# Kernel optimization log

Measured on AMD Instinct MI355X. Metric: run time of the kernel, lower is better.

The kernel has to match this reference:

```python
import jax, jax.numpy as jnp
import numpy as np

G = 4096              # number of graphs in batch
NPG = 198             # nodes per graph (fixed by view(-1, 198*2))
N = G * NPG           # total nodes = 811008
DEG = 8               # avg degree
E = N * DEG           # total edges = 6488064
CONV_DIMS = [(2, 20), (20, 15), (15, 10), (10, 5), (5, 2)]
MLP_DIMS = [(396, 200), (200, 100), (100, 50), (50, 10), (10, 2)]


def setup_inputs() -> dict:
    key = jax.random.key(0)
    ks = jax.random.split(key, 64)
    x = jax.random.normal(ks[0], (N, 2), dtype=jnp.float32)
    # block-diagonal edges: endpoints within each 198-node graph, then offset
    src = jax.random.randint(ks[1], (G, E // G), 0, NPG)
    dst = jax.random.randint(ks[2], (G, E // G), 0, NPG)
    off = (jnp.arange(G, dtype=jnp.int32) * NPG)[:, None]
    edge_index = jnp.stack([(src + off).reshape(-1), (dst + off).reshape(-1)]).astype(jnp.int32)
    edge_weight = jax.random.uniform(ks[3], (E,), dtype=jnp.float32)
    inp = {"x": x, "edge_index": edge_index, "edge_weight": edge_weight}
    ki = 4
    for i, (ci, co) in enumerate(CONV_DIMS):
        s = 1.0 / np.sqrt(ci)
        inp[f"w_rel{i}"] = jax.random.normal(ks[ki], (co, ci), jnp.float32) * s; ki += 1
        inp[f"b_rel{i}"] = jax.random.normal(ks[ki], (co,), jnp.float32) * s; ki += 1
        inp[f"w_root{i}"] = jax.random.normal(ks[ki], (co, ci), jnp.float32) * s; ki += 1
    for i, (ci, co) in enumerate(MLP_DIMS):
        s = 1.0 / np.sqrt(ci)
        inp[f"lw{i}"] = jax.random.normal(ks[ki], (co, ci), jnp.float32) * s; ki += 1
        inp[f"lb{i}"] = jax.random.normal(ks[ki], (co,), jnp.float32) * s; ki += 1
    return inp


def _graph_conv(x, src, dst, ew, w_rel, b_rel, w_root):
    # PyG GraphConv: lin_rel(sum_{j->i} e_ji * x_j) + lin_root(x_i)
    msg = x[src] * ew[:, None]                               # [E, Cin] gather
    agg = jax.ops.segment_sum(msg, dst, num_segments=N)      # [N, Cin] scatter-add
    return agg @ w_rel.T + b_rel + x @ w_root.T              # [N, Cout]


def reference(x, edge_index, edge_weight,
              w_rel0, b_rel0, w_root0, w_rel1, b_rel1, w_root1,
              w_rel2, b_rel2, w_root2, w_rel3, b_rel3, w_root3,
              w_rel4, b_rel4, w_root4,
              lw0, lb0, lw1, lb1, lw2, lb2, lw3, lb3, lw4, lb4):
    src, dst = edge_index[0], edge_index[1]
    convs = [(w_rel0, b_rel0, w_root0), (w_rel1, b_rel1, w_root1),
             (w_rel2, b_rel2, w_root2), (w_rel3, b_rel3, w_root3),
             (w_rel4, b_rel4, w_root4)]
    h = x
    for wr, br, wroot in convs:
        h = jax.nn.relu(_graph_conv(h, src, dst, edge_weight, wr, br, wroot))
    h = h.reshape(-1, NPG * 2)                               # [G, 396]
    mlp = [(lw0, lb0), (lw1, lb1), (lw2, lb2), (lw3, lb3)]
    for w, b in mlp:
        h = jax.nn.relu(h @ w.T + b)
    logits = h @ lw4.T + lb4                                 # [G, 2]
    return jax.nn.softmax(logits, axis=1)
```

## Files before the change

### kernel.cpp

```cpp
#include <hip/hip_runtime.h>
#include <hip/hip_fp16.h>

#define NG    4096
#define NPG   198
#define EPG   1584
#define ETOT  (NG * EPG)
#define SHW   12

#define BC2(u) __builtin_bit_cast(__half2, (u))

typedef _Float16 f16x4 __attribute__((ext_vector_type(4)));
typedef float    f32x4 __attribute__((ext_vector_type(4)));
typedef float    f32x2 __attribute__((ext_vector_type(2)));

#define H_F16S    (NG * 396)
#define WTB_SZ    114688
#define WTB1_OFF  83200
#define WTB2_OFF  106496
#define WTB3_OFF  113664
#define CPK_PAIRS 562

__global__ __launch_bounds__(256) void wtrans16_kernel(
    const float* __restrict__ w0, const float* __restrict__ w1,
    const float* __restrict__ w2, const float* __restrict__ w3,
    _Float16* __restrict__ wtb)
{
    const int idx = blockIdx.x * 256 + threadIdx.x;
    if (idx >= 2 * WTB_SZ) return;
    const int half = idx >= WTB_SZ;
    const int rel0 = idx - half * WTB_SZ;
    const float* w; int K, N, NPAD, rel;
    if (rel0 < 83200)       { w = w0; K = 396; N = 200; NPAD = 208; rel = rel0; }
    else if (rel0 < 106496) { w = w1; K = 200; N = 100; NPAD = 112; rel = rel0 - 83200; }
    else if (rel0 < 113664) { w = w2; K = 100; N = 50;  NPAD = 64;  rel = rel0 - 106496; }
    else                    { w = w3; K = 50;  N = 10;  NPAD = 16;  rel = rel0 - 113664; }
    const int span = NPAD * 16;
    const int kc = rel / span;
    const int r  = rel - kc * span;
    const int n  = r >> 4, ki = r & 15;
    const int k  = kc * 16 + ki;
    const float v = (n < N && k < K) ? w[n * K + k] : 0.f;
    const _Float16 hi = (_Float16)v;
    wtb[idx] = half ? (_Float16)(v - (float)hi) : hi;
}

__global__ __launch_bounds__(256) void wpackc_kernel(
    const float* wr0, const float* wq0, const float* wr1, const float* wq1,
    const float* wr2, const float* wq2, const float* wr3, const float* wq3,
    const float* wr4, const float* wq4, f32x2* __restrict__ cpk)
{
    const int idx = blockIdx.x * 256 + threadIdx.x;
    if (idx >= CPK_PAIRS) return;
    const float *wrel, *wroot; int COUT, CIN, MSP, base;
    if (idx < 40)       { wrel=wr0; wroot=wq0; COUT=20; CIN=2;  MSP=1;  base=0;   }
    else if (idx < 340) { wrel=wr1; wroot=wq1; COUT=15; CIN=20; MSP=10; base=40;  }
    else if (idx < 500) { wrel=wr2; wroot=wq2; COUT=10; CIN=15; MSP=8;  base=340; }
    else if (idx < 550) { wrel=wr3; wroot=wq3; COUT=5;  CIN=10; MSP=5;  base=500; }
    else                { wrel=wr4; wroot=wq4; COUT=2;  CIN=5;  MSP=3;  base=550; }
    const int r    = idx - base;
    const int half = r >= COUT * MSP;
    const int q    = r - half * COUT * MSP;
    const int o    = q / MSP, p = q - o * MSP;
    const float* w = half ? wroot : wrel;
    const int c0 = 2 * p, c1 = 2 * p + 1;
    f32x2 v;
    v.x = (c0 < CIN) ? w[o * CIN + c0] : 0.f;
    v.y = (c1 < CIN) ? w[o * CIN + c1] : 0.f;
    cpk[idx] = v;
}

template <int CIN, int COUT, int SIN, int SOUT>
__device__ __forceinline__ void conv_layer_h(
    const unsigned* __restrict__ h_in,
    unsigned* __restrict__ h_out,
    const unsigned* __restrict__ s_edge,
    const unsigned* __restrict__ row_start,
    const unsigned short* __restrict__ perm,
    const f32x2* __restrict__ wrelp,
    const f32x2* __restrict__ wrootp,
    const float* __restrict__ brel, int tid)
{
    if (tid >= NPG) return;
    const int node = (int)perm[tid];
    constexpr int MS = (CIN + 1) / 2;

    float aggf[MS * 2];
#pragma unroll
    for (int c = 0; c < MS * 2; ++c) aggf[c] = 0.f;

    const unsigned jb = row_start[node], je = row_start[node + 1];
    for (unsigned j = jb; j < je; ++j) {
        const unsigned e  = s_edge[j];
        const float    wf = __half2float(__ushort_as_half((unsigned short)(e >> 16)));
        const unsigned* row = h_in + (e & 0xFFFFu) * SIN;
        unsigned wv[MS];
        if constexpr (SIN == 1) {
            wv[0] = row[0];
        } else {
            const uint4 q0 = *(const uint4*)row;
            wv[0] = q0.x;
            if constexpr (MS > 1) wv[1] = q0.y;
            if constexpr (MS > 2) wv[2] = q0.z;
            if constexpr (MS > 3) wv[3] = q0.w;
            if constexpr (MS > 4) {
                const uint4 q1 = *(const uint4*)(row + 4);
                wv[4] = q1.x;
                if constexpr (MS > 5) wv[5] = q1.y;
                if constexpr (MS > 6) wv[6] = q1.z;
                if constexpr (MS > 7) wv[7] = q1.w;
            }
            if constexpr (MS > 8) {
                const uint4 q2 = *(const uint4*)(row + 8);
                wv[8] = q2.x;
                if constexpr (MS > 9) wv[9] = q2.y;
            }
        }
#pragma unroll
        for (int p = 0; p < MS; ++p) {
            const __half2 h2 = BC2(wv[p]);
            aggf[2*p]     = fmaf(wf, __low2float(h2),  aggf[2*p]);
            aggf[2*p + 1] = fmaf(wf, __high2float(h2), aggf[2*p + 1]);
        }
    }

    float hv[MS * 2];
    {
        const unsigned* me = h_in + node * SIN;
#pragma unroll
        for (int p = 0; p < MS; ++p) {
            const __half2 h2 = BC2(me[p]);
            hv[2*p]     = __low2float(h2);
            hv[2*p + 1] = __high2float(h2);
        }
    }

    float outv[COUT];
#pragma unroll
    for (int o = 0; o < COUT; ++o) {
        f32x2 acc; acc.x = brel[o]; acc.y = 0.f;
#pragma unroll
        for (int p = 0; p < MS; ++p) {
            f32x2 av; av.x = aggf[2*p]; av.y = aggf[2*p+1];
            acc = __builtin_elementwise_fma(av, wrelp[o * MS + p], acc);
            f32x2 hv2; hv2.x = hv[2*p]; hv2.y = hv[2*p+1];
            acc = __builtin_elementwise_fma(hv2, wrootp[o * MS + p], acc);
        }
        outv[o] = fmaxf(acc.x + acc.y, 0.f);
    }

    if constexpr (SOUT == 1) {
        h_out[node] = __builtin_bit_cast(unsigned,
            __floats2half2_rn(outv[0], COUT > 1 ? outv[1] : 0.f));
    } else {
        unsigned ow[SOUT];
#pragma unroll
        for (int p = 0; p < SOUT; ++p) {
            const float lo = (2 * p     < COUT) ? outv[2 * p]     : 0.f;
            const float hi = (2 * p + 1 < COUT) ? outv[2 * p + 1] : 0.f;
            ow[p] = __builtin_bit_cast(unsigned, __floats2half2_rn(lo, hi));
        }
        unsigned* orow = h_out + node * SOUT;
#pragma unroll
        for (int qn = 0; qn < SOUT / 4; ++qn)
            *(uint4*)(orow + 4 * qn) =
                make_uint4(ow[4*qn], ow[4*qn+1], ow[4*qn+2], ow[4*qn+3]);
    }
}

__global__ __launch_bounds__(256) void conv_kernel(
    const float* __restrict__ x,
    const int*   __restrict__ eidx,
    const float* __restrict__ ew,
    const f32x2* __restrict__ cpk,
    const float* __restrict__ br0, const float* __restrict__ br1,
    const float* __restrict__ br2, const float* __restrict__ br3,
    const float* __restrict__ br4,
    _Float16* __restrict__ H)
{
    __shared__ __align__(16) unsigned s_edge[EPG];
    __shared__ unsigned       cnt[256];
    __shared__ unsigned       cursor[256];
    __shared__ unsigned       row_start[NPG + 1];
    __shared__ unsigned       wsum[4];
    __shared__ unsigned       dhist[64];
    __shared__ unsigned       dcur[64];
    __shared__ unsigned short perm[NPG + 2];
    __shared__ __align__(16) unsigned bufA[NPG * SHW];
    __shared__ __align__(16) unsigned bufB[NPG * SHW];

    const int g = blockIdx.x, tid = threadIdx.x;
    const int ebase = g * EPG, nbase = g * NPG;
    const int lane = tid & 63, wid = tid >> 6;

    for (int i = tid; i < NPG * SHW; i += 256) { bufA[i] = 0u; bufB[i] = 0u; }

    const int4*   s4 = (const int4*)(eidx + ebase);
    const int4*   d4 = (const int4*)(eidx + ETOT + ebase);
    const float4* w4 = (const float4*)(ew + ebase);
    const int4   sa = s4[tid];
    const int4   da = d4[tid];
    const float4 wa = w4[tid];
    const bool hasb = tid < (EPG / 4 - 256);
    int4 sb = {0,0,0,0}, db = {0,0,0,0}; float4 wb = {0,0,0,0};
    if (hasb) { sb = s4[tid + 256]; db = d4[tid + 256]; wb = w4[tid + 256]; }

    cnt[tid] = 0u;
    __syncthreads();
    atomicAdd(&cnt[da.x - nbase], 1u); atomicAdd(&cnt[da.y - nbase], 1u);
    atomicAdd(&cnt[da.z - nbase], 1u); atomicAdd(&cnt[da.w - nbase], 1u);
    if (hasb) {
        atomicAdd(&cnt[db.x - nbase], 1u); atomicAdd(&cnt[db.y - nbase], 1u);
        atomicAdd(&cnt[db.z - nbase], 1u); atomicAdd(&cnt[db.w - nbase], 1u);
    }
    __syncthreads();

    const unsigned v = cnt[tid];
    unsigned inc = v;
#pragma unroll
    for (int s = 1; s < 64; s <<= 1) {
        const unsigned t = (unsigned)__shfl_up((int)inc, s);
        if (lane >= s) inc += t;
    }
    if (lane == 63) wsum[wid] = inc;
    __syncthreads();
    unsigned pre = 0;
    for (int w = 0; w < wid; ++w) pre += wsum[w];
    const unsigned excl = pre + inc - v;
    if (tid <= NPG) row_start[tid] = excl;
    if (tid < NPG)  cursor[tid]    = excl;
    __syncthreads();

    {
        auto place = [&](int s, int d, float w) {
            const int dl = d - nbase;
            const unsigned slot = atomicAdd(&cursor[dl], 1u);
            const __half hw = __float2half_rn(w);
            s_edge[slot] = ((unsigned)__half_as_ushort(hw) << 16)
                         | (unsigned)(s - nbase);
        };
        place(sa.x, da.x, wa.x); place(sa.y, da.y, wa.y);
        place(sa.z, da.z, wa.z); place(sa.w, da.w, wa.w);
        if (hasb) {
            place(sb.x, db.x, wb.x); place(sb.y, db.y, wb.y);
            place(sb.z, db.z, wb.z); place(sb.w, db.w, wb.w);
        }
    }

    if (tid < NPG) {
        const float2 xv = ((const float2*)x)[nbase + tid];
        bufA[tid] = __builtin_bit_cast(unsigned, __floats2half2_rn(xv.x, xv.y));
    }

    if (tid < 64) dhist[tid] = 0u;
    __syncthreads();
    unsigned mydeg = 0u;
    if (tid < NPG) {
        mydeg = v; if (mydeg > 63u) mydeg = 63u;
        atomicAdd(&dhist[mydeg], 1u);
    }
    __syncthreads();
    if (tid < 64) {
        const unsigned dv = dhist[tid];
        unsigned sc = dv;
#pragma unroll
        for (int s = 1; s < 64; s <<= 1) {
            const unsigned t = (unsigned)__shfl_up((int)sc, s);
            if (lane >= s) sc += t;
        }
        dcur[tid] = sc - dv;
    }
    __syncthreads();
    if (tid < NPG) {
        const unsigned pos = atomicAdd(&dcur[mydeg], 1u);
        perm[pos] = (unsigned short)tid;
    }
    __syncthreads();

    conv_layer_h<2,  20, 1,   SHW>(bufA, bufB, s_edge, row_start, perm,
                                   cpk + 0,   cpk + 20,        br0, tid);
    __syncthreads();
    conv_layer_h<20, 15, SHW, SHW>(bufB, bufA, s_edge, row_start, perm,
                                   cpk + 40,  cpk + 40 + 150,  br1, tid);
    __syncthreads();
    conv_layer_h<15, 10, SHW, SHW>(bufA, bufB, s_edge, row_start, perm,
                                   cpk + 340, cpk + 340 + 80,  br2, tid);
    __syncthreads();
    conv_layer_h<10, 5,  SHW, SHW>(bufB, bufA, s_edge, row_start, perm,
                                   cpk + 500, cpk + 500 + 25,  br3, tid);
    __syncthreads();
    conv_layer_h<5,  2,  SHW, 1  >(bufA, bufB, s_edge, row_start, perm,
                                   cpk + 550, cpk + 550 + 6,   br4, tid);
    __syncthreads();

    if (tid < NPG)
        ((unsigned*)H)[g * NPG + tid] = bufB[tid];
}

__device__ __forceinline__ void zero_words(void* p, int nwords, int tid)
{
    unsigned* u = (unsigned*)p;
    for (int i = tid; i < nwords; i += 512) u[i] = 0u;
}

template<int KC, int NTT, int NOUT, int SIN, int SOUT>
__device__ __forceinline__ void mfma_layer(
    const _Float16* __restrict__ inb,
    _Float16* __restrict__ outb,
    const _Float16* __restrict__ wthi,
    const _Float16* __restrict__ wtlo,
    const float* __restrict__ bias, int tid)
{
    constexpr int NPAD = NTT * 16;
    const int lane = tid & 63, wid = tid >> 6;
    const int lrow = lane & 15, lgrp = lane >> 4;
    const int nt0 = wid;
    if (nt0 >= NTT) return;
    const bool has2 = (nt0 + 8) < NTT;
    const _Float16* aptr = inb + lrow * SIN + lgrp * 4;

    f32x4 acc0 = {0.f, 0.f, 0.f, 0.f};
    f32x4 acc1 = {0.f, 0.f, 0.f, 0.f};
    const int n0 = nt0 * 16 + lrow;
    const int n1 = (nt0 + 8) * 16 + lrow;
    const int boff0 = n0 * 16 + lgrp * 4;
    const int boff1 = n1 * 16 + lgrp * 4;
#pragma unroll 4
    for (int kc = 0; kc < KC; ++kc) {
        const f16x4 a = *(const f16x4*)(aptr + kc * 16);
        const size_t kb = (size_t)kc * (NPAD * 16);
        acc0 = __builtin_amdgcn_mfma_f32_16x16x16f16(
            a, *(const f16x4*)(wthi + kb + boff0), acc0, 0, 0, 0);
        acc0 = __builtin_amdgcn_mfma_f32_16x16x16f16(
            a, *(const f16x4*)(wtlo + kb + boff0), acc0, 0, 0, 0);
        if (has2) {
            acc1 = __builtin_amdgcn_mfma_f32_16x16x16f16(
                a, *(const f16x4*)(wthi + kb + boff1), acc1, 0, 0, 0);
            acc1 = __builtin_amdgcn_mfma_f32_16x16x16f16(
                a, *(const f16x4*)(wtlo + kb + boff1), acc1, 0, 0, 0);
        }
    }
    if (n0 < NOUT) {
        const float bv = bias[n0];
#pragma unroll
        for (int j = 0; j < 4; ++j)
            outb[(lgrp * 4 + j) * SOUT + n0] = (_Float16)fmaxf(acc0[j] + bv, 0.f);
    }
    if (has2 && n1 < NOUT) {
        const float bv = bias[n1];
#pragma unroll
        for (int j = 0; j < 4; ++j)
            outb[(lgrp * 4 + j) * SOUT + n1] = (_Float16)fmaxf(acc1[j] + bv, 0.f);
    }
}

__global__ __launch_bounds__(512) void mlp_mfma_kernel(
    const _Float16* __restrict__ H,
    const _Float16* __restrict__ wtb,
    const float* __restrict__ lb0, const float* __restrict__ lb1,
    const float* __restrict__ lb2, const float* __restrict__ lb3,
    const float* __restrict__ lw4, const float* __restrict__ lb4,
    float* __restrict__ out)
{
    __shared__ __align__(16) _Float16 bufH[16 * 400];
    __shared__ __align__(16) _Float16 bufX[16 * 224];
    __shared__ __align__(16) _Float16 bufY[16 * 128];

    const int tid   = threadIdx.x;
    const int gbase = blockIdx.x * 16;
    const _Float16* lo = wtb + WTB_SZ;

    {
        const unsigned* Hw = (const unsigned*)H + (size_t)gbase * 198;
        unsigned* bH = (unsigned*)bufH;
        for (int t = tid; t < 16 * 200; t += 512) {
            const int gg = t / 200, w = t - gg * 200;
            bH[gg * 200 + w] = (w < 198) ? Hw[gg * 198 + w] : 0u;
        }
        zero_words(bufX, 16 * 224 / 2, tid);
        zero_words(bufY, 16 * 128 / 2, tid);
    }
    __syncthreads();

    mfma_layer<25, 13, 200, 400, 224>(bufH, bufX, wtb, lo, lb0, tid);
    __syncthreads();

    zero_words(bufH, 512, tid);
    mfma_layer<13, 7, 100, 224, 128>(bufX, bufY, wtb + WTB1_OFF, lo + WTB1_OFF, lb1, tid);
    __syncthreads();

    zero_words(bufX, 128, tid);
    mfma_layer<7, 4, 50, 128, 64>(bufY, bufH, wtb + WTB2_OFF, lo + WTB2_OFF, lb2, tid);
    __syncthreads();

    mfma_layer<4, 1, 10, 64, 16>(bufH, bufX, wtb + WTB3_OFF, lo + WTB3_OFF, lb3, tid);
    __syncthreads();

    if (tid < 16) {
        float l0 = lb4[0], l1 = lb4[1];
#pragma unroll
        for (int k = 0; k < 10; ++k) {
            const float hv = (float)bufX[tid * 16 + k];
            l0 = fmaf(hv, lw4[k],      l0);
            l1 = fmaf(hv, lw4[10 + k], l1);
        }
        const float m  = fmaxf(l0, l1);
        const float e0 = __expf(l0 - m), e1 = __expf(l1 - m);
        const float inv = 1.f / (e0 + e1);
        float2 p; p.x = e0 * inv; p.y = e1 * inv;
        ((float2*)out)[gbase + tid] = p;
    }
}

extern "C" void kernel_launch(void* const* d_in, const int* in_sizes, int n_in,
                              void* d_out, int out_size, void* d_ws, size_t ws_size,
                              hipStream_t stream)
{
    const float* x    = (const float*)d_in[0];
    const int*   eidx = (const int*)  d_in[1];
    const float* ew   = (const float*)d_in[2];

    const float* wr[5]; const float* br[5]; const float* wq[5];
    for (int i = 0; i < 5; ++i) {
        wr[i] = (const float*)d_in[3 + 3 * i];
        br[i] = (const float*)d_in[4 + 3 * i];
        wq[i] = (const float*)d_in[5 + 3 * i];
    }
    const float* lw[5]; const float* lb[5];
    for (int i = 0; i < 5; ++i) {
        lw[i] = (const float*)d_in[18 + 2 * i];
        lb[i] = (const float*)d_in[19 + 2 * i];
    }

    _Float16* wsH = (_Float16*)d_ws;
    _Float16* wtb = wsH + (size_t)H_F16S;
    f32x2*    cpk = (f32x2*)(wtb + (size_t)(2 * WTB_SZ));

    wtrans16_kernel<<<(2 * WTB_SZ + 255) / 256, 256, 0, stream>>>(
        lw[0], lw[1], lw[2], lw[3], wtb);

    wpackc_kernel<<<(CPK_PAIRS + 255) / 256, 256, 0, stream>>>(
        wr[0], wq[0], wr[1], wq[1], wr[2], wq[2], wr[3], wq[3], wr[4], wq[4],
        cpk);

    conv_kernel<<<NG, 256, 0, stream>>>(
        x, eidx, ew, cpk,
        br[0], br[1], br[2], br[3], br[4],
        wsH);

    mlp_mfma_kernel<<<NG / 16, 512, 0, stream>>>(
        wsH, wtb,
        lb[0], lb[1], lb[2], lb[3],
        lw[4], lb[4],
        (float*)d_out);
}
```

Baseline: 119.7 us.

## Merge weight-pack kernels, widen conv smem stride, halve MLP graphs per block

Merges the two weight-packing kernels into one launch. In the conv kernel, the feature row stride goes from 12 to 14 words with uint2 loads and stores, the buffer zeroing is dropped, row_start becomes 16-bit and the cursor array is removed by reusing cnt. The MLP kernel now handles 8 graphs per block instead of 16, doubling the grid while half of each MFMA tile is padding. This aims to cut launch overhead, reduce LDS bank conflicts and usage, and spread the MLP over more CUs, at the cost of wasted MFMA work and weight reloads.

```diff
diff --git a/kernel.cpp b/kernel.cpp
--- a/kernel.cpp
+++ b/kernel.cpp
@@ -5,7 +5,7 @@
 #define NPG   198
 #define EPG   1584
 #define ETOT  (NG * EPG)
-#define SHW   12
+#define SWW   14
 
 #define BC2(u) __builtin_bit_cast(__half2, (u))
 
@@ -20,44 +20,42 @@
 #define WTB3_OFF  113664
 #define CPK_PAIRS 562
 
-__global__ __launch_bounds__(256) void wtrans16_kernel(
+__global__ __launch_bounds__(256) void wpack_kernel(
     const float* __restrict__ w0, const float* __restrict__ w1,
     const float* __restrict__ w2, const float* __restrict__ w3,
-    _Float16* __restrict__ wtb)
-{
-    const int idx = blockIdx.x * 256 + threadIdx.x;
-    if (idx >= 2 * WTB_SZ) return;
-    const int half = idx >= WTB_SZ;
-    const int rel0 = idx - half * WTB_SZ;
-    const float* w; int K, N, NPAD, rel;
-    if (rel0 < 83200)       { w = w0; K = 396; N = 200; NPAD = 208; rel = rel0; }
-    else if (rel0 < 106496) { w = w1; K = 200; N = 100; NPAD = 112; rel = rel0 - 83200; }
-    else if (rel0 < 113664) { w = w2; K = 100; N = 50;  NPAD = 64;  rel = rel0 - 106496; }
-    else                    { w = w3; K = 50;  N = 10;  NPAD = 16;  rel = rel0 - 113664; }
-    const int span = NPAD * 16;
-    const int kc = rel / span;
-    const int r  = rel - kc * span;
-    const int n  = r >> 4, ki = r & 15;
-    const int k  = kc * 16 + ki;
-    const float v = (n < N && k < K) ? w[n * K + k] : 0.f;
-    const _Float16 hi = (_Float16)v;
-    wtb[idx] = half ? (_Float16)(v - (float)hi) : hi;
-}
-
-__global__ __launch_bounds__(256) void wpackc_kernel(
     const float* wr0, const float* wq0, const float* wr1, const float* wq1,
     const float* wr2, const float* wq2, const float* wr3, const float* wq3,
-    const float* wr4, const float* wq4, f32x2* __restrict__ cpk)
+    const float* wr4, const float* wq4,
+    _Float16* __restrict__ wtb, f32x2* __restrict__ cpk)
 {
     const int idx = blockIdx.x * 256 + threadIdx.x;
-    if (idx >= CPK_PAIRS) return;
+    if (idx < 2 * WTB_SZ) {
+        const int half = idx >= WTB_SZ;
+        const int rel0 = idx - half * WTB_SZ;
+        const float* w; int K, N, NPAD, rel;
+        if (rel0 < 83200)       { w = w0; K = 396; N = 200; NPAD = 208; rel = rel0; }
+        else if (rel0 < 106496) { w = w1; K = 200; N = 100; NPAD = 112; rel = rel0 - 83200; }
+        else if (rel0 < 113664) { w = w2; K = 100; N = 50;  NPAD = 64;  rel = rel0 - 106496; }
+        else                    { w = w3; K = 50;  N = 10;  NPAD = 16;  rel = rel0 - 113664; }
+        const int span = NPAD * 16;
+        const int kc = rel / span;
+        const int r  = rel - kc * span;
+        const int n  = r >> 4, ki = r & 15;
+        const int k  = kc * 16 + ki;
+        const float v = (n < N && k < K) ? w[n * K + k] : 0.f;
+        const _Float16 hi = (_Float16)v;
+        wtb[idx] = half ? (_Float16)(v - (float)hi) : hi;
+        return;
+    }
+    const int cidx = idx - 2 * WTB_SZ;
+    if (cidx >= CPK_PAIRS) return;
     const float *wrel, *wroot; int COUT, CIN, MSP, base;
-    if (idx < 40)       { wrel=wr0; wroot=wq0; COUT=20; CIN=2;  MSP=1;  base=0;   }
-    else if (idx < 340) { wrel=wr1; wroot=wq1; COUT=15; CIN=20; MSP=10; base=40;  }
-    else if (idx < 500) { wrel=wr2; wroot=wq2; COUT=10; CIN=15; MSP=8;  base=340; }
-    else if (idx < 550) { wrel=wr3; wroot=wq3; COUT=5;  CIN=10; MSP=5;  base=500; }
-    else                { wrel=wr4; wroot=wq4; COUT=2;  CIN=5;  MSP=3;  base=550; }
-    const int r    = idx - base;
+    if (cidx < 40)       { wrel=wr0; wroot=wq0; COUT=20; CIN=2;  MSP=1;  base=0;   }
+    else if (cidx < 340) { wrel=wr1; wroot=wq1; COUT=15; CIN=20; MSP=10; base=40;  }
+    else if (cidx < 500) { wrel=wr2; wroot=wq2; COUT=10; CIN=15; MSP=8;  base=340; }
+    else if (cidx < 550) { wrel=wr3; wroot=wq3; COUT=5;  CIN=10; MSP=5;  base=500; }
+    else                 { wrel=wr4; wroot=wq4; COUT=2;  CIN=5;  MSP=3;  base=550; }
+    const int r    = cidx - base;
     const int half = r >= COUT * MSP;
     const int q    = r - half * COUT * MSP;
     const int o    = q / MSP, p = q - o * MSP;
@@ -66,7 +64,7 @@
     f32x2 v;
     v.x = (c0 < CIN) ? w[o * CIN + c0] : 0.f;
     v.y = (c1 < CIN) ? w[o * CIN + c1] : 0.f;
-    cpk[idx] = v;
+    cpk[cidx] = v;
 }
 
 template <int CIN, int COUT, int SIN, int SOUT>
@@ -74,7 +72,7 @@
     const unsigned* __restrict__ h_in,
     unsigned* __restrict__ h_out,
     const unsigned* __restrict__ s_edge,
-    const unsigned* __restrict__ row_start,
+    const unsigned short* __restrict__ row_start,
     const unsigned short* __restrict__ perm,
     const f32x2* __restrict__ wrelp,
     const f32x2* __restrict__ wrootp,
@@ -97,23 +95,12 @@
         if constexpr (SIN == 1) {
             wv[0] = row[0];
         } else {
-            const uint4 q0 = *(const uint4*)row;
-            wv[0] = q0.x;
-            if constexpr (MS > 1) wv[1] = q0.y;
-            if constexpr (MS > 2) wv[2] = q0.z;
-            if constexpr (MS > 3) wv[3] = q0.w;
-            if constexpr (MS > 4) {
-                const uint4 q1 = *(const uint4*)(row + 4);
-                wv[4] = q1.x;
-                if constexpr (MS > 5) wv[5] = q1.y;
-                if constexpr (MS > 6) wv[6] = q1.z;
-                if constexpr (MS > 7) wv[7] = q1.w;
+#pragma unroll
+            for (int p = 0; p + 1 < MS; p += 2) {
+                const uint2 q = *(const uint2*)(row + p);
+                wv[p] = q.x; wv[p + 1] = q.y;
             }
-            if constexpr (MS > 8) {
-                const uint4 q2 = *(const uint4*)(row + 8);
-                wv[8] = q2.x;
-                if constexpr (MS > 9) wv[9] = q2.y;
-            }
+            if constexpr (MS & 1) wv[MS - 1] = row[MS - 1];
         }
 #pragma unroll
         for (int p = 0; p < MS; ++p) {
@@ -126,9 +113,20 @@
     float hv[MS * 2];
     {
         const unsigned* me = h_in + node * SIN;
+        unsigned mw[MS];
+        if constexpr (SIN == 1) {
+            mw[0] = me[0];
+        } else {
+#pragma unroll
+            for (int p = 0; p + 1 < MS; p += 2) {
+                const uint2 q = *(const uint2*)(me + p);
+                mw[p] = q.x; mw[p + 1] = q.y;
+            }
+            if constexpr (MS & 1) mw[MS - 1] = me[MS - 1];
+        }
 #pragma unroll
         for (int p = 0; p < MS; ++p) {
-            const __half2 h2 = BC2(me[p]);
+            const __half2 h2 = BC2(mw[p]);
             hv[2*p]     = __low2float(h2);
             hv[2*p + 1] = __high2float(h2);
         }
@@ -161,9 +159,8 @@
         }
         unsigned* orow = h_out + node * SOUT;
 #pragma unroll
-        for (int qn = 0; qn < SOUT / 4; ++qn)
-            *(uint4*)(orow + 4 * qn) =
-                make_uint4(ow[4*qn], ow[4*qn+1], ow[4*qn+2], ow[4*qn+3]);
+        for (int qn = 0; qn < SOUT; qn += 2)
+            *(uint2*)(orow + qn) = make_uint2(ow[qn], ow[qn + 1]);
     }
 }
 
@@ -179,20 +176,17 @@
 {
     __shared__ __align__(16) unsigned s_edge[EPG];
     __shared__ unsigned       cnt[256];
-    __shared__ unsigned       cursor[256];
-    __shared__ unsigned       row_start[NPG + 1];
+    __shared__ unsigned short row_start[NPG + 2];
     __shared__ unsigned       wsum[4];
     __shared__ unsigned       dhist[64];
     __shared__ unsigned       dcur[64];
     __shared__ unsigned short perm[NPG + 2];
-    __shared__ __align__(16) unsigned bufA[NPG * SHW];
-    __shared__ __align__(16) unsigned bufB[NPG * SHW];
+    __shared__ __align__(16) unsigned bufA[NPG * SWW];
+    __shared__ __align__(16) unsigned bufB[NPG * SWW];
 
     const int g = blockIdx.x, tid = threadIdx.x;
     const int ebase = g * EPG, nbase = g * NPG;
     const int lane = tid & 63, wid = tid >> 6;
-
-    for (int i = tid; i < NPG * SHW; i += 256) { bufA[i] = 0u; bufB[i] = 0u; }
 
     const int4*   s4 = (const int4*)(eidx + ebase);
     const int4*   d4 = (const int4*)(eidx + ETOT + ebase);
@@ -226,14 +220,14 @@
     unsigned pre = 0;
     for (int w = 0; w < wid; ++w) pre += wsum[w];
     const unsigned excl = pre + inc - v;
-    if (tid <= NPG) row_start[tid] = excl;
-    if (tid < NPG)  cursor[tid]    = excl;
+    if (tid <= NPG) row_start[tid] = (unsigned short)excl;
+    cnt[tid] = excl;
     __syncthreads();
 
     {
         auto place = [&](int s, int d, float w) {
             const int dl = d - nbase;
-            const unsigned slot = atomicAdd(&cursor[dl], 1u);
+            const unsigned slot = atomicAdd(&cnt[dl], 1u);
             const __half hw = __float2half_rn(w);
             s_edge[slot] = ((unsigned)__half_as_ushort(hw) << 16)
                          | (unsigned)(s - nbase);
@@ -276,19 +270,19 @@
     }
     __syncthreads();
 
-    conv_layer_h<2,  20, 1,   SHW>(bufA, bufB, s_edge, row_start, perm,
+    conv_layer_h<2,  20, 1,   SWW>(bufA, bufB, s_edge, row_start, perm,
                                    cpk + 0,   cpk + 20,        br0, tid);
     __syncthreads();
-    conv_layer_h<20, 15, SHW, SHW>(bufB, bufA, s_edge, row_start, perm,
+    conv_layer_h<20, 15, SWW, SWW>(bufB, bufA, s_edge, row_start, perm,
                                    cpk + 40,  cpk + 40 + 150,  br1, tid);
     __syncthreads();
-    conv_layer_h<15, 10, SHW, SHW>(bufA, bufB, s_edge, row_start, perm,
+    conv_layer_h<15, 10, SWW, SWW>(bufA, bufB, s_edge, row_start, perm,
                                    cpk + 340, cpk + 340 + 80,  br2, tid);
     __syncthreads();
-    conv_layer_h<10, 5,  SHW, SHW>(bufB, bufA, s_edge, row_start, perm,
+    conv_layer_h<10, 5,  SWW, SWW>(bufB, bufA, s_edge, row_start, perm,
                                    cpk + 500, cpk + 500 + 25,  br3, tid);
     __syncthreads();
-    conv_layer_h<5,  2,  SHW, 1  >(bufA, bufB, s_edge, row_start, perm,
+    conv_layer_h<5,  2,  SWW, 1  >(bufA, bufB, s_edge, row_start, perm,
                                    cpk + 550, cpk + 550 + 6,   br4, tid);
     __syncthreads();
 
@@ -366,7 +360,7 @@
     __shared__ __align__(16) _Float16 bufY[16 * 128];
 
     const int tid   = threadIdx.x;
-    const int gbase = blockIdx.x * 16;
+    const int gbase = blockIdx.x * 8;
     const _Float16* lo = wtb + WTB_SZ;
 
     {
@@ -374,7 +368,7 @@
         unsigned* bH = (unsigned*)bufH;
         for (int t = tid; t < 16 * 200; t += 512) {
             const int gg = t / 200, w = t - gg * 200;
-            bH[gg * 200 + w] = (w < 198) ? Hw[gg * 198 + w] : 0u;
+            bH[gg * 200 + w] = (gg < 8 && w < 198) ? Hw[gg * 198 + w] : 0u;
         }
         zero_words(bufX, 16 * 224 / 2, tid);
         zero_words(bufY, 16 * 128 / 2, tid);
@@ -395,7 +389,7 @@
     mfma_layer<4, 1, 10, 64, 16>(bufH, bufX, wtb + WTB3_OFF, lo + WTB3_OFF, lb3, tid);
     __syncthreads();
 
-    if (tid < 16) {
+    if (tid < 8) {
         float l0 = lb4[0], l1 = lb4[1];
 #pragma unroll
         for (int k = 0; k < 10; ++k) {
@@ -435,19 +429,18 @@
     _Float16* wtb = wsH + (size_t)H_F16S;
     f32x2*    cpk = (f32x2*)(wtb + (size_t)(2 * WTB_SZ));
 
-    wtrans16_kernel<<<(2 * WTB_SZ + 255) / 256, 256, 0, stream>>>(
-        lw[0], lw[1], lw[2], lw[3], wtb);
-
-    wpackc_kernel<<<(CPK_PAIRS + 255) / 256, 256, 0, stream>>>(
+    const int total_pack = 2 * WTB_SZ + CPK_PAIRS;
+    wpack_kernel<<<(total_pack + 255) / 256, 256, 0, stream>>>(
+        lw[0], lw[1], lw[2], lw[3],
         wr[0], wq[0], wr[1], wq[1], wr[2], wq[2], wr[3], wq[3], wr[4], wq[4],
-        cpk);
+        wtb, cpk);
 
     conv_kernel<<<NG, 256, 0, stream>>>(
         x, eidx, ew, cpk,
         br[0], br[1], br[2], br[3], br[4],
         wsH);
 
-    mlp_mfma_kernel<<<NG / 16, 512, 0, stream>>>(
+    mlp_mfma_kernel<<<NG / 8, 512, 0, stream>>>(
         wsH, wtb,
         lb[0], lb[1], lb[2], lb[3],
         lw[4], lb[4],
```

After: 121.5 us. Within noise of the previous version (+1.5%).
